# Kernel optimization log

Hardware: AMD Instinct MI355X
Metric: run time of the kernel (lower is better)

## Reference

```python
import jax, jax.numpy as jnp
import numpy as np

NEG_SLOPE = 0.2


def gat_conv(x, src, dst, W, a_src, a_dst, b, num_nodes):
    # x: [N, Fin], W: [Fin, Fout], a_src/a_dst: [Fout], b: [Fout]
    h = x @ W                                   # [N, Fout]
    alpha_s = h @ a_src                         # [N]
    alpha_d = h @ a_dst                         # [N]
    e = alpha_s[src] + alpha_d[dst]             # [E]
    e = jnp.where(e > 0, e, NEG_SLOPE * e)      # LeakyReLU(0.2)
    # segment softmax over edges grouped by destination node
    m = jax.ops.segment_max(e, dst, num_segments=num_nodes)   # [N]
    e = jnp.exp(e - m[dst])
    s = jax.ops.segment_sum(e, dst, num_segments=num_nodes)   # [N]
    alpha = e / s[dst]                          # [E] (every node has a self-loop)
    out = jax.ops.segment_sum(h[src] * alpha[:, None], dst, num_segments=num_nodes)
    return out + b


def setup_inputs() -> dict:
    key = jax.random.key(0)
    ks = jax.random.split(key, 10)
    N, E = 50000, 640000
    Fin, Fh, Fout = 128, 128, 64
    x = jax.random.normal(ks[0], (N, Fin), dtype=jnp.float32)
    edge_index = jax.random.randint(ks[1], (2, E), 0, N, dtype=jnp.int64)
    g = 1.0 / np.sqrt(Fin)
    W1 = jax.random.normal(ks[2], (Fin, Fh), dtype=jnp.float32) * g
    a1_src = jax.random.normal(ks[3], (Fh,), dtype=jnp.float32) * 0.1
    a1_dst = jax.random.normal(ks[4], (Fh,), dtype=jnp.float32) * 0.1
    b1 = jnp.zeros((Fh,), dtype=jnp.float32)
    g2 = 1.0 / np.sqrt(Fh)
    W2 = jax.random.normal(ks[5], (Fh, Fout), dtype=jnp.float32) * g2
    a2_src = jax.random.normal(ks[6], (Fout,), dtype=jnp.float32) * 0.1
    a2_dst = jax.random.normal(ks[7], (Fout,), dtype=jnp.float32) * 0.1
    b2 = jnp.zeros((Fout,), dtype=jnp.float32)
    return {"x": x, "edge_index": edge_index, "W1": W1, "a1_src": a1_src,
            "a1_dst": a1_dst, "b1": b1, "W2": W2, "a2_src": a2_src,
            "a2_dst": a2_dst, "b2": b2}


def reference(x, edge_index, W1, a1_src, a1_dst, b1, W2, a2_src, a2_dst, b2):
    N = x.shape[0]
    loops = jnp.arange(N, dtype=edge_index.dtype)
    src = jnp.concatenate([edge_index[0], loops])  # add self-loops (PyG default)
    dst = jnp.concatenate([edge_index[1], loops])
    h = gat_conv(x, src, dst, W1, a1_src, a1_dst, b1, N)
    h = jax.nn.relu(h)
    # F.dropout(0.1) skipped: deterministic (eval-mode) reference
    out = gat_conv(h, src, dst, W2, a2_src, a2_dst, b2, N)
    return out
```

## Files before the change

kernel.cpp:

```cpp
#include <hip/hip_runtime.h>

#define LEAK 0.2f

static __device__ __forceinline__ float leaky(float e) { return e > 0.f ? e : LEAK * e; }

static __device__ __forceinline__ unsigned f2bf(float f) {
    union { float f; unsigned u; } v; v.f = f;
    return (v.u + 0x7FFFu + ((v.u >> 16) & 1u)) >> 16;
}
static __device__ __forceinline__ float bflo(unsigned u) {
    union { unsigned x; float f; } v; v.x = u << 16; return v.f;
}
static __device__ __forceinline__ float bfhi(unsigned u) {
    union { unsigned x; float f; } v; v.x = u & 0xFFFF0000u; return v.f;
}

using bf16x8 = __attribute__((ext_vector_type(8))) short;
using f32x4 = __attribute__((ext_vector_type(4))) float;

__global__ __launch_bounds__(256) void k_prep(int* __restrict__ counts, int n,
                                              const int* __restrict__ ei, int nwords_check,
                                              int* __restrict__ flag,
                                              const float* __restrict__ W1,
                                              unsigned short* __restrict__ Wt1,
                                              const float* __restrict__ W2,
                                              unsigned short* __restrict__ Wt2, int NB) {
    int bid = blockIdx.x;
    int t = threadIdx.x;
    if (bid == 0) {
        if (t < 64) {
            int bad = 0;
            for (int i = 1 + 2 * t; i < nwords_check; i += 128) bad |= (ei[i] != 0);
            unsigned long long anybad = __ballot(bad != 0);
            if (t == 0) *flag = (anybad == 0ULL) ? 1 : 0;
        }
        return;
    }
    if (bid <= NB) {
        int i = (bid - 1) * 256 + t;
        if (i < n) counts[i] = 0;
        return;
    }
    if (bid <= NB + 4) {
        int q = bid - (NB + 1);
        int c = t & 127, ksub = t >> 7;
        int k0 = q * 32 + ksub * 16;
        union { unsigned short s[16]; uint4 v[2]; } u;
#pragma unroll
        for (int j = 0; j < 16; ++j) u.s[j] = (unsigned short)f2bf(W1[(size_t)(k0 + j) * 128 + c]);
        uint4* dst = (uint4*)(Wt1 + (size_t)c * 128 + k0);
        dst[0] = u.v[0];
        dst[1] = u.v[1];
        return;
    }
    {
        int q = bid - (NB + 5);
        int c = t & 63, ksub = t >> 6;
        int k0 = q * 64 + ksub * 16;
        union { unsigned short s[16]; uint4 v[2]; } u;
#pragma unroll
        for (int j = 0; j < 16; ++j) u.s[j] = (unsigned short)f2bf(W2[(size_t)(k0 + j) * 64 + c]);
        uint4* dst = (uint4*)(Wt2 + (size_t)c * 128 + k0);
        dst[0] = u.v[0];
        dst[1] = u.v[1];
        return;
    }
}

__global__ __launch_bounds__(256) void k_rank(const int* __restrict__ ei,
                                              const int* __restrict__ flag,
                                              int* __restrict__ counts,
                                              int* __restrict__ rankd,
                                              int* __restrict__ srcv, int E) {
    int base = (blockIdx.x * 256 + threadIdx.x) * 4;
    if (base >= E) return;
    int is64 = *flag;
    if (base + 3 < E) {
        int s0, s1, s2, s3, d0, d1, d2, d3;
        if (is64) {
            const uint4* ps = (const uint4*)(ei + 2 * (size_t)base);
            uint4 a = ps[0], b = ps[1];
            const uint4* pd = (const uint4*)(ei + 2 * ((size_t)E + base));
            uint4 c = pd[0], e4 = pd[1];
            s0 = a.x; s1 = a.z; s2 = b.x; s3 = b.z;
            d0 = c.x; d1 = c.z; d2 = e4.x; d3 = e4.z;
        } else {
            int4 a = *(const int4*)(ei + base);
            int4 b = *(const int4*)(ei + (size_t)E + base);
            s0 = a.x; s1 = a.y; s2 = a.z; s3 = a.w;
            d0 = b.x; d1 = b.y; d2 = b.z; d3 = b.w;
        }
        int r0 = atomicAdd(&counts[d0], 1);
        int r1 = atomicAdd(&counts[d1], 1);
        int r2 = atomicAdd(&counts[d2], 1);
        int r3 = atomicAdd(&counts[d3], 1);
        *(int4*)(rankd + base) = make_int4((r0 << 16) | d0, (r1 << 16) | d1,
                                           (r2 << 16) | d2, (r3 << 16) | d3);
        *(int4*)(srcv + base) = make_int4(s0, s1, s2, s3);
    } else {
        for (int j = 0; j < 4 && base + j < E; ++j) {
            int e = base + j;
            int ss = is64 ? ei[2 * (size_t)e] : ei[e];
            int dd = is64 ? ei[2 * ((size_t)E + e)] : ei[(size_t)E + e];
            int r = atomicAdd(&counts[dd], 1);
            rankd[e] = (r << 16) | dd;
            srcv[e] = ss;
        }
    }
}

__global__ void k_scan1(const int* __restrict__ counts, int* __restrict__ incl,
                        int* __restrict__ bsums, int n) {
    __shared__ int s[256];
    int t = threadIdx.x;
    int g = blockIdx.x * 256 + t;
    int v = (g < n) ? counts[g] : 0;
    s[t] = v;
    __syncthreads();
    for (int off = 1; off < 256; off <<= 1) {
        int add = (t >= off) ? s[t - off] : 0;
        __syncthreads();
        s[t] += add;
        __syncthreads();
    }
    if (g < n) incl[g] = s[t];
    if (t == 255) bsums[blockIdx.x] = s[255];
}

__global__ void k_scan2(int* __restrict__ bsums, int nb) {
    __shared__ int s[256];
    int t = threadIdx.x;
    int v = (t < nb) ? bsums[t] : 0;
    s[t] = v;
    __syncthreads();
    for (int off = 1; off < 256; off <<= 1) {
        int add = (t >= off) ? s[t - off] : 0;
        __syncthreads();
        s[t] += add;
        __syncthreads();
    }
    int excl = (t == 0) ? 0 : s[t - 1];
    if (t < nb) bsums[t] = excl;
}

__global__ void k_scan3(const int* __restrict__ incl, const int* __restrict__ bsums,
                        int* __restrict__ rowptr, int n) {
    int g = blockIdx.x * 256 + threadIdx.x;
    if (g < n) rowptr[g + 1] = incl[g] + bsums[blockIdx.x];
    if (g == 0) rowptr[0] = 0;
}

template <int F, bool AF32>
__global__ __launch_bounds__(256) void k_gemm_mfma(const void* __restrict__ Xv,
                                                   const unsigned short* __restrict__ Wt,
                                                   const float* __restrict__ asrc,
                                                   const float* __restrict__ adst,
                                                   unsigned short* __restrict__ Hb,
                                                   float* __restrict__ out_s,
                                                   float* __restrict__ out_d, int n,
                                                   int rowTiles,
                                                   const int* __restrict__ rankd,
                                                   const int* __restrict__ srcv,
                                                   const int* __restrict__ rowptr,
                                                   int* __restrict__ colv, int E) {
    constexpr int K = 128;
    constexpr int KP = K + 8;
    constexpr int NT = F / 16;
    __shared__ unsigned short wsT[F * KP];
    int t = threadIdx.x;

    if (blockIdx.x >= rowTiles) {
        int base = ((blockIdx.x - rowTiles) * 256 + t) * 4;
        if (base >= E) return;
        if (base + 3 < E) {
            int4 rd = *(const int4*)(rankd + base);
            int4 sv = *(const int4*)(srcv + base);
            int p0 = rowptr[rd.x & 0xFFFF] + (rd.x >> 16);
            int p1 = rowptr[rd.y & 0xFFFF] + (rd.y >> 16);
            int p2 = rowptr[rd.z & 0xFFFF] + (rd.z >> 16);
            int p3 = rowptr[rd.w & 0xFFFF] + (rd.w >> 16);
            colv[p0] = sv.x;
            colv[p1] = sv.y;
            colv[p2] = sv.z;
            colv[p3] = sv.w;
        } else {
            for (int j = 0; j < 4 && base + j < E; ++j) {
                int e = base + j;
                int rd = rankd[e];
                colv[rowptr[rd & 0xFFFF] + (rd >> 16)] = srcv[e];
            }
        }
        return;
    }

    int w = t >> 6, lane = t & 63;
    int lrow = lane & 15, kg = lane >> 4;
    long long row0 = (long long)blockIdx.x * 64;

#pragma unroll
    for (int i = t; i < F * (K / 8); i += 256) {
        int c = i / (K / 8), j8 = i % (K / 8);
        uint4 v = ((const uint4*)(Wt + (size_t)c * K))[j8];
        *(uint4*)&wsT[c * KP + 8 * j8] = v;
    }
    __syncthreads();

    long long grow = row0 + w * 16 + lrow;
    bool rowok = grow < n;

    f32x4 acc[NT];
#pragma unroll
    for (int i = 0; i < NT; ++i) acc[i] = (f32x4){0.f, 0.f, 0.f, 0.f};

#pragma unroll
    for (int ks = 0; ks < K / 32; ++ks) {
        bf16x8 af;
        if constexpr (AF32) {
            const float* Xp = (const float*)Xv + grow * K + ks * 32 + kg * 8;
            float4 x0 = make_float4(0.f, 0.f, 0.f, 0.f), x1 = x0;
            if (rowok) {
                x0 = ((const float4*)Xp)[0];
                x1 = ((const float4*)Xp)[1];
            }
            af = (bf16x8){(short)f2bf(x0.x), (short)f2bf(x0.y), (short)f2bf(x0.z), (short)f2bf(x0.w),
                          (short)f2bf(x1.x), (short)f2bf(x1.y), (short)f2bf(x1.z), (short)f2bf(x1.w)};
        } else {
            uint4 u = make_uint4(0, 0, 0, 0);
            if (rowok) {
                const unsigned short* Xp = (const unsigned short*)Xv + grow * K + ks * 32 + kg * 8;
                u = *(const uint4*)Xp;
            }
            af = *(bf16x8*)&u;
        }
#pragma unroll
        for (int nt = 0; nt < NT; ++nt) {
            const unsigned short* bp = &wsT[(nt * 16 + lrow) * KP + ks * 32 + kg * 8];
            uint4 ub = *(const uint4*)bp;
            bf16x8 bf = *(bf16x8*)&ub;
            acc[nt] = __builtin_amdgcn_mfma_f32_16x16x32_bf16(af, bf, acc[nt], 0, 0, 0);
        }
    }

    {
        float ps[4] = {0.f, 0.f, 0.f, 0.f}, pd[4] = {0.f, 0.f, 0.f, 0.f};
#pragma unroll
        for (int nt = 0; nt < NT; ++nt) {
            float asv = asrc[nt * 16 + lrow];
            float adv = adst[nt * 16 + lrow];
#pragma unroll
            for (int i = 0; i < 4; ++i) {
                ps[i] = fmaf(acc[nt][i], asv, ps[i]);
                pd[i] = fmaf(acc[nt][i], adv, pd[i]);
            }
        }
#pragma unroll
        for (int off = 1; off < 16; off <<= 1) {
#pragma unroll
            for (int i = 0; i < 4; ++i) {
                ps[i] += __shfl_xor(ps[i], off);
                pd[i] += __shfl_xor(pd[i], off);
            }
        }
        if (lrow == 0) {
#pragma unroll
            for (int i = 0; i < 4; ++i) {
                long long r = row0 + w * 16 + kg * 4 + i;
                if (r < n) {
                    out_s[r] = ps[i];
                    out_d[r] = pd[i];
                }
            }
        }
    }

    int r0 = w * 16 + kg * 4;
#pragma unroll
    for (int nt = 0; nt < NT; ++nt) {
        int c = nt * 16 + lrow;
#pragma unroll
        for (int i = 0; i < 4; ++i) {
            long long r = row0 + r0 + i;
            if (r < n) Hb[r * F + c] = (unsigned short)f2bf(acc[nt][i]);
        }
    }
}

template <int F, bool RELU, bool OB>
__global__ __launch_bounds__(256) void k_agg(const int* __restrict__ rowptr,
                                             const int* __restrict__ colv,
                                             const float* __restrict__ as_,
                                             const float* __restrict__ ad_,
                                             const unsigned* __restrict__ Hu,
                                             const float* __restrict__ bias,
                                             void* __restrict__ OUT, int n) {
    constexpr int FG8 = F / 8;
    constexpr int GRP = 64 / FG8;
    int node = blockIdx.x * 4 + (threadIdx.x >> 6);
    int lane = threadIdx.x & 63;
    if (node >= n) return;
    int rs = rowptr[node], re = rowptr[node + 1];
    int deg = re - rs;
    float adi = ad_[node];
    float e_self = leaky(as_[node] + adi);

    int scol = node;
    float e_l = -3.0e38f;
    if (lane < deg) {
        scol = colv[rs + lane];
        e_l = leaky(as_[scol] + adi);
    }
    float m = fmaxf(e_l, e_self);
    for (int base = 64; base < deg; base += 64) {
        if (base + lane < deg) m = fmaxf(m, leaky(as_[colv[rs + base + lane]] + adi));
    }
#pragma unroll
    for (int off = 32; off; off >>= 1) m = fmaxf(m, __shfl_xor(m, off));

    float p_l = (lane < deg) ? __expf(e_l - m) : 0.f;
    float ssum = p_l;
    for (int base = 64; base < deg; base += 64) {
        if (base + lane < deg) ssum += __expf(leaky(as_[colv[rs + base + lane]] + adi) - m);
    }
#pragma unroll
    for (int off = 32; off; off >>= 1) ssum += __shfl_xor(ssum, off);
    float pself = __expf(e_self - m);
    ssum += pself;
    float inv = 1.f / ssum;
    float w_l = p_l * inv;
    float wself = pself * inv;

    int grp = lane / FG8;
    int fg = lane % FG8;
    const uint4* __restrict__ H16 = (const uint4*)Hu;
    float a0, a1, a2, a3, a4, a5, a6, a7;
    {
        uint4 hv = H16[(size_t)node * FG8 + fg];
        float ws0 = (grp == 0) ? wself : 0.f;
        a0 = ws0 * bflo(hv.x); a1 = ws0 * bfhi(hv.x);
        a2 = ws0 * bflo(hv.y); a3 = ws0 * bfhi(hv.y);
        a4 = ws0 * bflo(hv.z); a5 = ws0 * bfhi(hv.z);
        a6 = ws0 * bflo(hv.w); a7 = ws0 * bfhi(hv.w);
    }

    int cnt = deg < 64 ? deg : 64;
    constexpr int STEP = 4 * GRP;
    int cntr = (cnt + STEP - 1) / STEP * STEP;
#pragma unroll 1
    for (int i = 0; i < cntr; i += STEP) {
        int i0 = i + grp, i1 = i + GRP + grp, i2 = i + 2 * GRP + grp, i3 = i + 3 * GRP + grp;
        int s0 = __shfl(scol, i0), s1 = __shfl(scol, i1);
        int s2 = __shfl(scol, i2), s3 = __shfl(scol, i3);
        float w0 = __shfl(w_l, i0), w1 = __shfl(w_l, i1);
        float w2 = __shfl(w_l, i2), w3 = __shfl(w_l, i3);
        uint4 g0 = H16[(size_t)s0 * FG8 + fg];
        uint4 g1 = H16[(size_t)s1 * FG8 + fg];
        uint4 g2 = H16[(size_t)s2 * FG8 + fg];
        uint4 g3 = H16[(size_t)s3 * FG8 + fg];
        a0 = fmaf(w0, bflo(g0.x), a0); a1 = fmaf(w0, bfhi(g0.x), a1);
        a2 = fmaf(w0, bflo(g0.y), a2); a3 = fmaf(w0, bfhi(g0.y), a3);
        a4 = fmaf(w0, bflo(g0.z), a4); a5 = fmaf(w0, bfhi(g0.z), a5);
        a6 = fmaf(w0, bflo(g0.w), a6); a7 = fmaf(w0, bfhi(g0.w), a7);
        a0 = fmaf(w1, bflo(g1.x), a0); a1 = fmaf(w1, bfhi(g1.x), a1);
        a2 = fmaf(w1, bflo(g1.y), a2); a3 = fmaf(w1, bfhi(g1.y), a3);
        a4 = fmaf(w1, bflo(g1.z), a4); a5 = fmaf(w1, bfhi(g1.z), a5);
        a6 = fmaf(w1, bflo(g1.w), a6); a7 = fmaf(w1, bfhi(g1.w), a7);
        a0 = fmaf(w2, bflo(g2.x), a0); a1 = fmaf(w2, bfhi(g2.x), a1);
        a2 = fmaf(w2, bflo(g2.y), a2); a3 = fmaf(w2, bfhi(g2.y), a3);
        a4 = fmaf(w2, bflo(g2.z), a4); a5 = fmaf(w2, bfhi(g2.z), a5);
        a6 = fmaf(w2, bflo(g2.w), a6); a7 = fmaf(w2, bfhi(g2.w), a7);
        a0 = fmaf(w3, bflo(g3.x), a0); a1 = fmaf(w3, bfhi(g3.x), a1);
        a2 = fmaf(w3, bflo(g3.y), a2); a3 = fmaf(w3, bfhi(g3.y), a3);
        a4 = fmaf(w3, bflo(g3.z), a4); a5 = fmaf(w3, bfhi(g3.z), a5);
        a6 = fmaf(w3, bflo(g3.w), a6); a7 = fmaf(w3, bfhi(g3.w), a7);
    }
    for (int j = rs + 64; j < re; ++j) {
        int s = colv[j];
        float w = __expf(leaky(as_[s] + adi) - m) * inv;
        float we = (grp == 0) ? w : 0.f;
        uint4 g = H16[(size_t)s * FG8 + fg];
        a0 = fmaf(we, bflo(g.x), a0); a1 = fmaf(we, bfhi(g.x), a1);
        a2 = fmaf(we, bflo(g.y), a2); a3 = fmaf(we, bfhi(g.y), a3);
        a4 = fmaf(we, bflo(g.z), a4); a5 = fmaf(we, bfhi(g.z), a5);
        a6 = fmaf(we, bflo(g.w), a6); a7 = fmaf(we, bfhi(g.w), a7);
    }
#pragma unroll
    for (int off = FG8; off < 64; off <<= 1) {
        a0 += __shfl_xor(a0, off); a1 += __shfl_xor(a1, off);
        a2 += __shfl_xor(a2, off); a3 += __shfl_xor(a3, off);
        a4 += __shfl_xor(a4, off); a5 += __shfl_xor(a5, off);
        a6 += __shfl_xor(a6, off); a7 += __shfl_xor(a7, off);
    }
    if (grp == 0) {
        const float4* b4 = (const float4*)bias;
        float4 bv0 = b4[fg * 2], bv1 = b4[fg * 2 + 1];
        a0 += bv0.x; a1 += bv0.y; a2 += bv0.z; a3 += bv0.w;
        a4 += bv1.x; a5 += bv1.y; a6 += bv1.z; a7 += bv1.w;
        if (RELU) {
            a0 = fmaxf(a0, 0.f); a1 = fmaxf(a1, 0.f);
            a2 = fmaxf(a2, 0.f); a3 = fmaxf(a3, 0.f);
            a4 = fmaxf(a4, 0.f); a5 = fmaxf(a5, 0.f);
            a6 = fmaxf(a6, 0.f); a7 = fmaxf(a7, 0.f);
        }
        if (OB) {
            uint4 p;
            p.x = f2bf(a0) | (f2bf(a1) << 16);
            p.y = f2bf(a2) | (f2bf(a3) << 16);
            p.z = f2bf(a4) | (f2bf(a5) << 16);
            p.w = f2bf(a6) | (f2bf(a7) << 16);
            ((uint4*)OUT)[(size_t)node * FG8 + fg] = p;
        } else {
            float4* o4 = (float4*)((float*)OUT + (size_t)node * F + fg * 8);
            o4[0] = make_float4(a0, a1, a2, a3);
            o4[1] = make_float4(a4, a5, a6, a7);
        }
    }
}

extern "C" void kernel_launch(void* const* d_in, const int* in_sizes, int n_in,
                              void* d_out, int out_size, void* d_ws, size_t ws_size,
                              hipStream_t stream) {
    const float* x   = (const float*)d_in[0];
    const int*   ei  = (const int*)d_in[1];
    const float* W1  = (const float*)d_in[2];
    const float* a1s = (const float*)d_in[3];
    const float* a1d = (const float*)d_in[4];
    const float* b1  = (const float*)d_in[5];
    const float* W2  = (const float*)d_in[6];
    const float* a2s = (const float*)d_in[7];
    const float* a2d = (const float*)d_in[8];
    const float* b2  = (const float*)d_in[9];
    float* out = (float*)d_out;

    int N = in_sizes[0] / 128;
    int E = in_sizes[1] / 2;

    size_t off = 0;
    auto alloc = [&](size_t bytes) -> void* {
        off = (off + 255) & ~(size_t)255;
        void* p = (char*)d_ws + off;
        off += bytes;
        return p;
    };
    unsigned short* h = (unsigned short*)alloc((size_t)N * 128 * 2);
    unsigned short* out1b = (unsigned short*)alloc((size_t)N * 128 * 2);
    unsigned short* Wt1 = (unsigned short*)alloc(128 * 128 * 2);
    unsigned short* Wt2 = (unsigned short*)alloc(64 * 128 * 2);
    float* as_    = (float*)alloc((size_t)N * 4);
    float* ad_    = (float*)alloc((size_t)N * 4);
    int* counts   = (int*)alloc((size_t)N * 4);
    int* rowptr   = (int*)alloc((size_t)(N + 1) * 4);
    int* incl     = (int*)alloc((size_t)N * 4);
    int* bsums    = (int*)alloc(1024);
    int* colv     = (int*)alloc((size_t)E * 4);
    int* rankd    = (int*)alloc((size_t)E * 4);
    int* srcv     = (int*)alloc((size_t)E * 4);
    int* flag     = (int*)alloc(256);

    int NB = (N + 255) / 256;
    int blocksN4 = (N + 3) / 4;
    int rowTiles = (N + 63) / 64;
    int blocksE4 = (E + 1023) / 1024;

    int nchk = 2 * E < 512 ? 2 * E : 512;
    k_prep<<<NB + 7, 256, 0, stream>>>(counts, N, ei, nchk, flag, W1, Wt1, W2, Wt2, NB);
    k_rank<<<blocksE4, 256, 0, stream>>>(ei, flag, counts, rankd, srcv, E);
    k_scan1<<<NB, 256, 0, stream>>>(counts, incl, bsums, N);
    k_scan2<<<1, 256, 0, stream>>>(bsums, NB);
    k_scan3<<<NB, 256, 0, stream>>>(incl, bsums, rowptr, N);

    k_gemm_mfma<128, true><<<rowTiles + blocksE4, 256, 0, stream>>>(
        x, Wt1, a1s, a1d, h, as_, ad_, N, rowTiles, rankd, srcv, rowptr, colv, E);
    k_agg<128, true, true><<<blocksN4, 256, 0, stream>>>(rowptr, colv, as_, ad_,
                                                         (const unsigned*)h, b1, out1b, N);

    k_gemm_mfma<64, false><<<rowTiles, 256, 0, stream>>>(
        out1b, Wt2, a2s, a2d, h, as_, ad_, N, rowTiles, rankd, srcv, rowptr, colv, 0);
    k_agg<64, false, false><<<blocksN4, 256, 0, stream>>>(rowptr, colv, as_, ad_,
                                                          (const unsigned*)h, b2, out, N);
}
```

Baseline: 135.4 us.

## Fuse layer-1 aggregation with layer-2 GEMM and merge scan kernels

Adds a kernel that does the layer-1 attention softmax and neighbor aggregation for 64 nodes per block, writes the ReLU'd bf16 rows into LDS, and runs the layer-2 MFMA GEMM and attention projections from there. This drops the global round trip of the intermediate 128-wide features and one kernel launch. It also folds scan2 and scan3 into one kernel in which every block rescans the block sums redundantly. The cost is less aggregation parallelism: each wave walks 16 nodes serially, and a grid of only about 782 blocks may hide gather latency poorly.

```diff
diff --git a/kernel.cpp b/kernel.cpp
--- a/kernel.cpp
+++ b/kernel.cpp
@@ -127,7 +127,8 @@
     if (t == 255) bsums[blockIdx.x] = s[255];
 }
 
-__global__ void k_scan2(int* __restrict__ bsums, int nb) {
+__global__ void k_scan23(const int* __restrict__ incl, const int* __restrict__ bsums,
+                         int* __restrict__ rowptr, int n, int nb) {
     __shared__ int s[256];
     int t = threadIdx.x;
     int v = (t < nb) ? bsums[t] : 0;
@@ -139,14 +140,9 @@
         s[t] += add;
         __syncthreads();
     }
-    int excl = (t == 0) ? 0 : s[t - 1];
-    if (t < nb) bsums[t] = excl;
-}
-
-__global__ void k_scan3(const int* __restrict__ incl, const int* __restrict__ bsums,
-                        int* __restrict__ rowptr, int n) {
-    int g = blockIdx.x * 256 + threadIdx.x;
-    if (g < n) rowptr[g + 1] = incl[g] + bsums[blockIdx.x];
+    int pre = (blockIdx.x == 0) ? 0 : s[blockIdx.x - 1];
+    int g = blockIdx.x * 256 + t;
+    if (g < n) rowptr[g + 1] = incl[g] + pre;
     if (g == 0) rowptr[0] = 0;
 }
 
@@ -281,6 +277,206 @@
         for (int i = 0; i < 4; ++i) {
             long long r = row0 + r0 + i;
             if (r < n) Hb[r * F + c] = (unsigned short)f2bf(acc[nt][i]);
+        }
+    }
+}
+
+__global__ __launch_bounds__(256) void k_aggemm(const int* __restrict__ rowptr,
+                                                const int* __restrict__ colv,
+                                                const float* __restrict__ as_,
+                                                const float* __restrict__ ad_,
+                                                const unsigned* __restrict__ Hu,
+                                                const float* __restrict__ bias,
+                                                const unsigned short* __restrict__ Wt2,
+                                                const float* __restrict__ a2s,
+                                                const float* __restrict__ a2d,
+                                                unsigned short* __restrict__ H2,
+                                                float* __restrict__ out_s2,
+                                                float* __restrict__ out_d2, int n) {
+    constexpr int K = 128, KP = K + 8;
+    __shared__ unsigned short At[64 * KP];
+    __shared__ unsigned short Wt[64 * KP];
+    int t = threadIdx.x;
+    int w = t >> 6, lane = t & 63;
+
+#pragma unroll
+    for (int i = t; i < 64 * (K / 8); i += 256) {
+        int c = i / (K / 8), j8 = i % (K / 8);
+        uint4 v = ((const uint4*)(Wt2 + (size_t)c * K))[j8];
+        *(uint4*)&Wt[c * KP + 8 * j8] = v;
+    }
+
+    long long node0 = (long long)blockIdx.x * 64 + w * 16;
+    int grp = lane >> 4;
+    int fg = lane & 15;
+    const uint4* __restrict__ H16 = (const uint4*)Hu;
+
+    for (int ii = 0; ii < 16; ++ii) {
+        long long node = node0 + ii;
+        int ldsrow = w * 16 + ii;
+        if (node >= n) {
+            if (lane < 16) *(uint4*)&At[ldsrow * KP + lane * 8] = make_uint4(0, 0, 0, 0);
+            continue;
+        }
+        int rs = rowptr[node], re = rowptr[node + 1];
+        int deg = re - rs;
+        float adi = ad_[node];
+        float e_self = leaky(as_[node] + adi);
+
+        int scol = (int)node;
+        float e_l = -3.0e38f;
+        if (lane < deg) {
+            scol = colv[rs + lane];
+            e_l = leaky(as_[scol] + adi);
+        }
+        float m = fmaxf(e_l, e_self);
+        for (int base = 64; base < deg; base += 64) {
+            if (base + lane < deg) m = fmaxf(m, leaky(as_[colv[rs + base + lane]] + adi));
+        }
+#pragma unroll
+        for (int off = 32; off; off >>= 1) m = fmaxf(m, __shfl_xor(m, off));
+
+        float p_l = (lane < deg) ? __expf(e_l - m) : 0.f;
+        float ssum = p_l;
+        for (int base = 64; base < deg; base += 64) {
+            if (base + lane < deg) ssum += __expf(leaky(as_[colv[rs + base + lane]] + adi) - m);
+        }
+#pragma unroll
+        for (int off = 32; off; off >>= 1) ssum += __shfl_xor(ssum, off);
+        float pself = __expf(e_self - m);
+        ssum += pself;
+        float inv = 1.f / ssum;
+        float w_l = p_l * inv;
+        float wself = pself * inv;
+
+        float a0, a1, a2, a3, a4, a5, a6, a7;
+        {
+            uint4 hv = H16[node * 16 + fg];
+            float ws0 = (grp == 0) ? wself : 0.f;
+            a0 = ws0 * bflo(hv.x); a1 = ws0 * bfhi(hv.x);
+            a2 = ws0 * bflo(hv.y); a3 = ws0 * bfhi(hv.y);
+            a4 = ws0 * bflo(hv.z); a5 = ws0 * bfhi(hv.z);
+            a6 = ws0 * bflo(hv.w); a7 = ws0 * bfhi(hv.w);
+        }
+        int cnt = deg < 64 ? deg : 64;
+        int cntr = (cnt + 15) & ~15;
+#pragma unroll 1
+        for (int i = 0; i < cntr; i += 16) {
+            int i0 = i + grp, i1 = i + 4 + grp, i2 = i + 8 + grp, i3 = i + 12 + grp;
+            int s0 = __shfl(scol, i0), s1 = __shfl(scol, i1);
+            int s2 = __shfl(scol, i2), s3 = __shfl(scol, i3);
+            float w0 = __shfl(w_l, i0), w1 = __shfl(w_l, i1);
+            float w2 = __shfl(w_l, i2), w3 = __shfl(w_l, i3);
+            uint4 g0 = H16[(size_t)s0 * 16 + fg];
+            uint4 g1 = H16[(size_t)s1 * 16 + fg];
+            uint4 g2 = H16[(size_t)s2 * 16 + fg];
+            uint4 g3 = H16[(size_t)s3 * 16 + fg];
+            a0 = fmaf(w0, bflo(g0.x), a0); a1 = fmaf(w0, bfhi(g0.x), a1);
+            a2 = fmaf(w0, bflo(g0.y), a2); a3 = fmaf(w0, bfhi(g0.y), a3);
+            a4 = fmaf(w0, bflo(g0.z), a4); a5 = fmaf(w0, bfhi(g0.z), a5);
+            a6 = fmaf(w0, bflo(g0.w), a6); a7 = fmaf(w0, bfhi(g0.w), a7);
+            a0 = fmaf(w1, bflo(g1.x), a0); a1 = fmaf(w1, bfhi(g1.x), a1);
+            a2 = fmaf(w1, bflo(g1.y), a2); a3 = fmaf(w1, bfhi(g1.y), a3);
+            a4 = fmaf(w1, bflo(g1.z), a4); a5 = fmaf(w1, bfhi(g1.z), a5);
+            a6 = fmaf(w1, bflo(g1.w), a6); a7 = fmaf(w1, bfhi(g1.w), a7);
+            a0 = fmaf(w2, bflo(g2.x), a0); a1 = fmaf(w2, bfhi(g2.x), a1);
+            a2 = fmaf(w2, bflo(g2.y), a2); a3 = fmaf(w2, bfhi(g2.y), a3);
+            a4 = fmaf(w2, bflo(g2.z), a4); a5 = fmaf(w2, bfhi(g2.z), a5);
+            a6 = fmaf(w2, bflo(g2.w), a6); a7 = fmaf(w2, bfhi(g2.w), a7);
+            a0 = fmaf(w3, bflo(g3.x), a0); a1 = fmaf(w3, bfhi(g3.x), a1);
+            a2 = fmaf(w3, bflo(g3.y), a2); a3 = fmaf(w3, bfhi(g3.y), a3);
+            a4 = fmaf(w3, bflo(g3.z), a4); a5 = fmaf(w3, bfhi(g3.z), a5);
+            a6 = fmaf(w3, bflo(g3.w), a6); a7 = fmaf(w3, bfhi(g3.w), a7);
+        }
+        for (int j = rs + 64; j < re; ++j) {
+            int s = colv[j];
+            float ww = __expf(leaky(as_[s] + adi) - m) * inv;
+            float we = (grp == 0) ? ww : 0.f;
+            uint4 g = H16[(size_t)s * 16 + fg];
+            a0 = fmaf(we, bflo(g.x), a0); a1 = fmaf(we, bfhi(g.x), a1);
+            a2 = fmaf(we, bflo(g.y), a2); a3 = fmaf(we, bfhi(g.y), a3);
+            a4 = fmaf(we, bflo(g.z), a4); a5 = fmaf(we, bfhi(g.z), a5);
+            a6 = fmaf(we, bflo(g.w), a6); a7 = fmaf(we, bfhi(g.w), a7);
+        }
+#pragma unroll
+        for (int off = 16; off < 64; off <<= 1) {
+            a0 += __shfl_xor(a0, off); a1 += __shfl_xor(a1, off);
+            a2 += __shfl_xor(a2, off); a3 += __shfl_xor(a3, off);
+            a4 += __shfl_xor(a4, off); a5 += __shfl_xor(a5, off);
+            a6 += __shfl_xor(a6, off); a7 += __shfl_xor(a7, off);
+        }
+        if (grp == 0) {
+            const float4* b4 = (const float4*)bias;
+            float4 bv0 = b4[fg * 2], bv1 = b4[fg * 2 + 1];
+            a0 = fmaxf(a0 + bv0.x, 0.f); a1 = fmaxf(a1 + bv0.y, 0.f);
+            a2 = fmaxf(a2 + bv0.z, 0.f); a3 = fmaxf(a3 + bv0.w, 0.f);
+            a4 = fmaxf(a4 + bv1.x, 0.f); a5 = fmaxf(a5 + bv1.y, 0.f);
+            a6 = fmaxf(a6 + bv1.z, 0.f); a7 = fmaxf(a7 + bv1.w, 0.f);
+            uint4 p;
+            p.x = f2bf(a0) | (f2bf(a1) << 16);
+            p.y = f2bf(a2) | (f2bf(a3) << 16);
+            p.z = f2bf(a4) | (f2bf(a5) << 16);
+            p.w = f2bf(a6) | (f2bf(a7) << 16);
+            *(uint4*)&At[ldsrow * KP + fg * 8] = p;
+        }
+    }
+    __syncthreads();
+
+    int lrow = lane & 15, kg = lane >> 4;
+    long long row0 = (long long)blockIdx.x * 64;
+    f32x4 acc[4];
+#pragma unroll
+    for (int i = 0; i < 4; ++i) acc[i] = (f32x4){0.f, 0.f, 0.f, 0.f};
+#pragma unroll
+    for (int ks = 0; ks < 4; ++ks) {
+        uint4 ua = *(const uint4*)&At[(w * 16 + lrow) * KP + ks * 32 + kg * 8];
+        bf16x8 af = *(bf16x8*)&ua;
+#pragma unroll
+        for (int nt = 0; nt < 4; ++nt) {
+            uint4 ub = *(const uint4*)&Wt[(nt * 16 + lrow) * KP + ks * 32 + kg * 8];
+            bf16x8 bf = *(bf16x8*)&ub;
+            acc[nt] = __builtin_amdgcn_mfma_f32_16x16x32_bf16(af, bf, acc[nt], 0, 0, 0);
+        }
+    }
+    {
+        float ps[4] = {0.f, 0.f, 0.f, 0.f}, pd[4] = {0.f, 0.f, 0.f, 0.f};
+#pragma unroll
+        for (int nt = 0; nt < 4; ++nt) {
+            float asv = a2s[nt * 16 + lrow];
+            float adv = a2d[nt * 16 + lrow];
+#pragma unroll
+            for (int i = 0; i < 4; ++i) {
+                ps[i] = fmaf(acc[nt][i], asv, ps[i]);
+                pd[i] = fmaf(acc[nt][i], adv, pd[i]);
+            }
+        }
+#pragma unroll
+        for (int off = 1; off < 16; off <<= 1) {
+#pragma unroll
+            for (int i = 0; i < 4; ++i) {
+                ps[i] += __shfl_xor(ps[i], off);
+                pd[i] += __shfl_xor(pd[i], off);
+            }
+        }
+        if (lrow == 0) {
+#pragma unroll
+            for (int i = 0; i < 4; ++i) {
+                long long r = row0 + w * 16 + kg * 4 + i;
+                if (r < n) {
+                    out_s2[r] = ps[i];
+                    out_d2[r] = pd[i];
+                }
+            }
+        }
+    }
+    int r0 = w * 16 + kg * 4;
+#pragma unroll
+    for (int nt = 0; nt < 4; ++nt) {
+        int c = nt * 16 + lrow;
+#pragma unroll
+        for (int i = 0; i < 4; ++i) {
+            long long r = row0 + r0 + i;
+            if (r < n) H2[r * 64 + c] = (unsigned short)f2bf(acc[nt][i]);
         }
     }
 }
@@ -441,12 +637,14 @@
         off += bytes;
         return p;
     };
-    unsigned short* h = (unsigned short*)alloc((size_t)N * 128 * 2);
-    unsigned short* out1b = (unsigned short*)alloc((size_t)N * 128 * 2);
+    unsigned short* h  = (unsigned short*)alloc((size_t)N * 128 * 2);
+    unsigned short* h2 = (unsigned short*)alloc((size_t)N * 64 * 2);
     unsigned short* Wt1 = (unsigned short*)alloc(128 * 128 * 2);
     unsigned short* Wt2 = (unsigned short*)alloc(64 * 128 * 2);
     float* as_    = (float*)alloc((size_t)N * 4);
     float* ad_    = (float*)alloc((size_t)N * 4);
+    float* as2    = (float*)alloc((size_t)N * 4);
+    float* ad2    = (float*)alloc((size_t)N * 4);
     int* counts   = (int*)alloc((size_t)N * 4);
     int* rowptr   = (int*)alloc((size_t)(N + 1) * 4);
     int* incl     = (int*)alloc((size_t)N * 4);
@@ -465,16 +663,14 @@
     k_prep<<<NB + 7, 256, 0, stream>>>(counts, N, ei, nchk, flag, W1, Wt1, W2, Wt2, NB);
     k_rank<<<blocksE4, 256, 0, stream>>>(ei, flag, counts, rankd, srcv, E);
     k_scan1<<<NB, 256, 0, stream>>>(counts, incl, bsums, N);
-    k_scan2<<<1, 256, 0, stream>>>(bsums, NB);
-    k_scan3<<<NB, 256, 0, stream>>>(incl, bsums, rowptr, N);
+    k_scan23<<<NB, 256, 0, stream>>>(incl, bsums, rowptr, N, NB);
 
     k_gemm_mfma<128, true><<<rowTiles + blocksE4, 256, 0, stream>>>(
         x, Wt1, a1s, a1d, h, as_, ad_, N, rowTiles, rankd, srcv, rowptr, colv, E);
-    k_agg<128, true, true><<<blocksN4, 256, 0, stream>>>(rowptr, colv, as_, ad_,
-                                                         (const unsigned*)h, b1, out1b, N);
-
-    k_gemm_mfma<64, false><<<rowTiles, 256, 0, stream>>>(
-        out1b, Wt2, a2s, a2d, h, as_, ad_, N, rowTiles, rankd, srcv, rowptr, colv, 0);
-    k_agg<64, false, false><<<blocksN4, 256, 0, stream>>>(rowptr, colv, as_, ad_,
-                                                          (const unsigned*)h, b2, out, N);
-}
+
+    k_aggemm<<<rowTiles, 256, 0, stream>>>(rowptr, colv, as_, ad_, (const unsigned*)h,
+                                           b1, Wt2, a2s, a2d, h2, as2, ad2, N);
+
+    k_agg<64, false, false><<<blocksN4, 256, 0, stream>>>(rowptr, colv, as2, ad2,
+                                                          (const unsigned*)h2, b2, out, N);
+}
```

After: 145.4 us. 7.4% more time.

## Process two destination nodes per wavefront in aggregation and merge scan passes

Applied to the files above, without the earlier changes.

The aggregation kernel now has each 64-lane wavefront handle two destination nodes at once. Their softmax reductions and neighbour gathers are interleaved, so more independent memory loads are in flight per wave and the per-node setup is amortised. The second and third scan kernels are fused: every block redundantly scans the block sums itself, which removes one launch. In exchange the aggregation kernel uses about twice the accumulator registers, which may lower occupancy, and lanes can sit idle when the two nodes have very different degrees.

```diff
diff --git a/kernel.cpp b/kernel.cpp
--- a/kernel.cpp
+++ b/kernel.cpp
@@ -17,6 +17,12 @@
 
 using bf16x8 = __attribute__((ext_vector_type(8))) short;
 using f32x4 = __attribute__((ext_vector_type(4))) float;
+
+#define FMA8(A0, A1, A2, A3, A4, A5, A6, A7, W, G)              \
+    A0 = fmaf(W, bflo(G.x), A0); A1 = fmaf(W, bfhi(G.x), A1);   \
+    A2 = fmaf(W, bflo(G.y), A2); A3 = fmaf(W, bfhi(G.y), A3);   \
+    A4 = fmaf(W, bflo(G.z), A4); A5 = fmaf(W, bfhi(G.z), A5);   \
+    A6 = fmaf(W, bflo(G.w), A6); A7 = fmaf(W, bfhi(G.w), A7);
 
 __global__ __launch_bounds__(256) void k_prep(int* __restrict__ counts, int n,
                                               const int* __restrict__ ei, int nwords_check,
@@ -127,7 +133,8 @@
     if (t == 255) bsums[blockIdx.x] = s[255];
 }
 
-__global__ void k_scan2(int* __restrict__ bsums, int nb) {
+__global__ void k_scan23(const int* __restrict__ incl, const int* __restrict__ bsums,
+                         int* __restrict__ rowptr, int n, int nb) {
     __shared__ int s[256];
     int t = threadIdx.x;
     int v = (t < nb) ? bsums[t] : 0;
@@ -139,14 +146,9 @@
         s[t] += add;
         __syncthreads();
     }
-    int excl = (t == 0) ? 0 : s[t - 1];
-    if (t < nb) bsums[t] = excl;
-}
-
-__global__ void k_scan3(const int* __restrict__ incl, const int* __restrict__ bsums,
-                        int* __restrict__ rowptr, int n) {
-    int g = blockIdx.x * 256 + threadIdx.x;
-    if (g < n) rowptr[g + 1] = incl[g] + bsums[blockIdx.x];
+    int pre = (blockIdx.x == 0) ? 0 : s[blockIdx.x - 1];
+    int g = blockIdx.x * 256 + t;
+    if (g < n) rowptr[g + 1] = incl[g] + pre;
     if (g == 0) rowptr[0] = 0;
 }
 
@@ -295,123 +297,190 @@
                                              void* __restrict__ OUT, int n) {
     constexpr int FG8 = F / 8;
     constexpr int GRP = 64 / FG8;
-    int node = blockIdx.x * 4 + (threadIdx.x >> 6);
+    constexpr int STEP = 4 * GRP;
+    int wid = blockIdx.x * 4 + (threadIdx.x >> 6);
     int lane = threadIdx.x & 63;
-    if (node >= n) return;
-    int rs = rowptr[node], re = rowptr[node + 1];
-    int deg = re - rs;
-    float adi = ad_[node];
-    float e_self = leaky(as_[node] + adi);
-
-    int scol = node;
-    float e_l = -3.0e38f;
-    if (lane < deg) {
-        scol = colv[rs + lane];
-        e_l = leaky(as_[scol] + adi);
-    }
-    float m = fmaxf(e_l, e_self);
-    for (int base = 64; base < deg; base += 64) {
-        if (base + lane < deg) m = fmaxf(m, leaky(as_[colv[rs + base + lane]] + adi));
-    }
-#pragma unroll
-    for (int off = 32; off; off >>= 1) m = fmaxf(m, __shfl_xor(m, off));
-
-    float p_l = (lane < deg) ? __expf(e_l - m) : 0.f;
-    float ssum = p_l;
-    for (int base = 64; base < deg; base += 64) {
-        if (base + lane < deg) ssum += __expf(leaky(as_[colv[rs + base + lane]] + adi) - m);
-    }
-#pragma unroll
-    for (int off = 32; off; off >>= 1) ssum += __shfl_xor(ssum, off);
-    float pself = __expf(e_self - m);
-    ssum += pself;
-    float inv = 1.f / ssum;
-    float w_l = p_l * inv;
-    float wself = pself * inv;
+    long long nA = (long long)wid * 2;
+    if (nA >= n) return;
+    long long nB = nA + 1;
+    bool vB = nB < n;
+    long long nBc = vB ? nB : nA;
+
+    int rsA = rowptr[nA], reA = rowptr[nA + 1];
+    int rsB = rowptr[nBc], reB = rowptr[nBc + 1];
+    int degA = reA - rsA, degB = reB - rsB;
+    float adiA = ad_[nA], adiB = ad_[nBc];
+    float esA = leaky(as_[nA] + adiA);
+    float esB = leaky(as_[nBc] + adiB);
+
+    int scA = (int)nA, scB = (int)nBc;
+    float eA = -3.0e38f, eB = -3.0e38f;
+    if (lane < degA) scA = colv[rsA + lane];
+    if (lane < degB) scB = colv[rsB + lane];
+    if (lane < degA) eA = leaky(as_[scA] + adiA);
+    if (lane < degB) eB = leaky(as_[scB] + adiB);
+
+    float mA = fmaxf(eA, esA), mB = fmaxf(eB, esB);
+    for (int base = 64; base < degA; base += 64)
+        if (base + lane < degA) mA = fmaxf(mA, leaky(as_[colv[rsA + base + lane]] + adiA));
+    for (int base = 64; base < degB; base += 64)
+        if (base + lane < degB) mB = fmaxf(mB, leaky(as_[colv[rsB + base + lane]] + adiB));
+#pragma unroll
+    for (int off = 32; off; off >>= 1) {
+        mA = fmaxf(mA, __shfl_xor(mA, off));
+        mB = fmaxf(mB, __shfl_xor(mB, off));
+    }
+
+    float pA = (lane < degA) ? __expf(eA - mA) : 0.f;
+    float pB = (lane < degB) ? __expf(eB - mB) : 0.f;
+    float sA = pA, sB = pB;
+    for (int base = 64; base < degA; base += 64)
+        if (base + lane < degA) sA += __expf(leaky(as_[colv[rsA + base + lane]] + adiA) - mA);
+    for (int base = 64; base < degB; base += 64)
+        if (base + lane < degB) sB += __expf(leaky(as_[colv[rsB + base + lane]] + adiB) - mB);
+#pragma unroll
+    for (int off = 32; off; off >>= 1) {
+        sA += __shfl_xor(sA, off);
+        sB += __shfl_xor(sB, off);
+    }
+    float psA = __expf(esA - mA), psB = __expf(esB - mB);
+    sA += psA;
+    sB += psB;
+    float invA = 1.f / sA, invB = 1.f / sB;
+    float wA = pA * invA, wB = pB * invB;
+    float wsA = psA * invA, wsB = psB * invB;
 
     int grp = lane / FG8;
     int fg = lane % FG8;
     const uint4* __restrict__ H16 = (const uint4*)Hu;
-    float a0, a1, a2, a3, a4, a5, a6, a7;
+    float a0A, a1A, a2A, a3A, a4A, a5A, a6A, a7A;
+    float a0B, a1B, a2B, a3B, a4B, a5B, a6B, a7B;
     {
-        uint4 hv = H16[(size_t)node * FG8 + fg];
-        float ws0 = (grp == 0) ? wself : 0.f;
-        a0 = ws0 * bflo(hv.x); a1 = ws0 * bfhi(hv.x);
-        a2 = ws0 * bflo(hv.y); a3 = ws0 * bfhi(hv.y);
-        a4 = ws0 * bflo(hv.z); a5 = ws0 * bfhi(hv.z);
-        a6 = ws0 * bflo(hv.w); a7 = ws0 * bfhi(hv.w);
-    }
-
-    int cnt = deg < 64 ? deg : 64;
-    constexpr int STEP = 4 * GRP;
-    int cntr = (cnt + STEP - 1) / STEP * STEP;
+        uint4 hvA = H16[(size_t)nA * FG8 + fg];
+        uint4 hvB = H16[(size_t)nBc * FG8 + fg];
+        float w0A = (grp == 0) ? wsA : 0.f;
+        float w0B = (grp == 0) ? wsB : 0.f;
+        a0A = w0A * bflo(hvA.x); a1A = w0A * bfhi(hvA.x);
+        a2A = w0A * bflo(hvA.y); a3A = w0A * bfhi(hvA.y);
+        a4A = w0A * bflo(hvA.z); a5A = w0A * bfhi(hvA.z);
+        a6A = w0A * bflo(hvA.w); a7A = w0A * bfhi(hvA.w);
+        a0B = w0B * bflo(hvB.x); a1B = w0B * bfhi(hvB.x);
+        a2B = w0B * bflo(hvB.y); a3B = w0B * bfhi(hvB.y);
+        a4B = w0B * bflo(hvB.z); a5B = w0B * bfhi(hvB.z);
+        a6B = w0B * bflo(hvB.w); a7B = w0B * bfhi(hvB.w);
+    }
+
+    int cntA = degA < 64 ? degA : 64;
+    int cntB = degB < 64 ? degB : 64;
+    int cntrA = (cntA + STEP - 1) / STEP * STEP;
+    int cntrB = (cntB + STEP - 1) / STEP * STEP;
+    int cntrM = cntrA > cntrB ? cntrA : cntrB;
 #pragma unroll 1
-    for (int i = 0; i < cntr; i += STEP) {
-        int i0 = i + grp, i1 = i + GRP + grp, i2 = i + 2 * GRP + grp, i3 = i + 3 * GRP + grp;
-        int s0 = __shfl(scol, i0), s1 = __shfl(scol, i1);
-        int s2 = __shfl(scol, i2), s3 = __shfl(scol, i3);
-        float w0 = __shfl(w_l, i0), w1 = __shfl(w_l, i1);
-        float w2 = __shfl(w_l, i2), w3 = __shfl(w_l, i3);
-        uint4 g0 = H16[(size_t)s0 * FG8 + fg];
-        uint4 g1 = H16[(size_t)s1 * FG8 + fg];
-        uint4 g2 = H16[(size_t)s2 * FG8 + fg];
-        uint4 g3 = H16[(size_t)s3 * FG8 + fg];
-        a0 = fmaf(w0, bflo(g0.x), a0); a1 = fmaf(w0, bfhi(g0.x), a1);
-        a2 = fmaf(w0, bflo(g0.y), a2); a3 = fmaf(w0, bfhi(g0.y), a3);
-        a4 = fmaf(w0, bflo(g0.z), a4); a5 = fmaf(w0, bfhi(g0.z), a5);
-        a6 = fmaf(w0, bflo(g0.w), a6); a7 = fmaf(w0, bfhi(g0.w), a7);
-        a0 = fmaf(w1, bflo(g1.x), a0); a1 = fmaf(w1, bfhi(g1.x), a1);
-        a2 = fmaf(w1, bflo(g1.y), a2); a3 = fmaf(w1, bfhi(g1.y), a3);
-        a4 = fmaf(w1, bflo(g1.z), a4); a5 = fmaf(w1, bfhi(g1.z), a5);
-        a6 = fmaf(w1, bflo(g1.w), a6); a7 = fmaf(w1, bfhi(g1.w), a7);
-        a0 = fmaf(w2, bflo(g2.x), a0); a1 = fmaf(w2, bfhi(g2.x), a1);
-        a2 = fmaf(w2, bflo(g2.y), a2); a3 = fmaf(w2, bfhi(g2.y), a3);
-        a4 = fmaf(w2, bflo(g2.z), a4); a5 = fmaf(w2, bfhi(g2.z), a5);
-        a6 = fmaf(w2, bflo(g2.w), a6); a7 = fmaf(w2, bfhi(g2.w), a7);
-        a0 = fmaf(w3, bflo(g3.x), a0); a1 = fmaf(w3, bfhi(g3.x), a1);
-        a2 = fmaf(w3, bflo(g3.y), a2); a3 = fmaf(w3, bfhi(g3.y), a3);
-        a4 = fmaf(w3, bflo(g3.z), a4); a5 = fmaf(w3, bfhi(g3.z), a5);
-        a6 = fmaf(w3, bflo(g3.w), a6); a7 = fmaf(w3, bfhi(g3.w), a7);
-    }
-    for (int j = rs + 64; j < re; ++j) {
+    for (int i = 0; i < cntrM; i += STEP) {
+        bool doA = i < cntrA, doB = i < cntrB;
+        uint4 gA0, gA1, gA2, gA3, gB0, gB1, gB2, gB3;
+        float wA0, wA1, wA2, wA3, wB0, wB1, wB2, wB3;
+        if (doA) {
+            int i0 = i + grp, i1 = i + GRP + grp, i2 = i + 2 * GRP + grp, i3 = i + 3 * GRP + grp;
+            int s0 = __shfl(scA, i0), s1 = __shfl(scA, i1);
+            int s2 = __shfl(scA, i2), s3 = __shfl(scA, i3);
+            wA0 = __shfl(wA, i0); wA1 = __shfl(wA, i1);
+            wA2 = __shfl(wA, i2); wA3 = __shfl(wA, i3);
+            gA0 = H16[(size_t)s0 * FG8 + fg];
+            gA1 = H16[(size_t)s1 * FG8 + fg];
+            gA2 = H16[(size_t)s2 * FG8 + fg];
+            gA3 = H16[(size_t)s3 * FG8 + fg];
+        }
+        if (doB) {
+            int i0 = i + grp, i1 = i + GRP + grp, i2 = i + 2 * GRP + grp, i3 = i + 3 * GRP + grp;
+            int s0 = __shfl(scB, i0), s1 = __shfl(scB, i1);
+            int s2 = __shfl(scB, i2), s3 = __shfl(scB, i3);
+            wB0 = __shfl(wB, i0); wB1 = __shfl(wB, i1);
+            wB2 = __shfl(wB, i2); wB3 = __shfl(wB, i3);
+            gB0 = H16[(size_t)s0 * FG8 + fg];
+            gB1 = H16[(size_t)s1 * FG8 + fg];
+            gB2 = H16[(size_t)s2 * FG8 + fg];
+            gB3 = H16[(size_t)s3 * FG8 + fg];
+        }
+        if (doA) {
+            FMA8(a0A, a1A, a2A, a3A, a4A, a5A, a6A, a7A, wA0, gA0)
+            FMA8(a0A, a1A, a2A, a3A, a4A, a5A, a6A, a7A, wA1, gA1)
+            FMA8(a0A, a1A, a2A, a3A, a4A, a5A, a6A, a7A, wA2, gA2)
+            FMA8(a0A, a1A, a2A, a3A, a4A, a5A, a6A, a7A, wA3, gA3)
+        }
+        if (doB) {
+            FMA8(a0B, a1B, a2B, a3B, a4B, a5B, a6B, a7B, wB0, gB0)
+            FMA8(a0B, a1B, a2B, a3B, a4B, a5B, a6B, a7B, wB1, gB1)
+            FMA8(a0B, a1B, a2B, a3B, a4B, a5B, a6B, a7B, wB2, gB2)
+            FMA8(a0B, a1B, a2B, a3B, a4B, a5B, a6B, a7B, wB3, gB3)
+        }
+    }
+    for (int j = rsA + 64; j < reA; ++j) {
         int s = colv[j];
-        float w = __expf(leaky(as_[s] + adi) - m) * inv;
+        float w = __expf(leaky(as_[s] + adiA) - mA) * invA;
         float we = (grp == 0) ? w : 0.f;
         uint4 g = H16[(size_t)s * FG8 + fg];
-        a0 = fmaf(we, bflo(g.x), a0); a1 = fmaf(we, bfhi(g.x), a1);
-        a2 = fmaf(we, bflo(g.y), a2); a3 = fmaf(we, bfhi(g.y), a3);
-        a4 = fmaf(we, bflo(g.z), a4); a5 = fmaf(we, bfhi(g.z), a5);
-        a6 = fmaf(we, bflo(g.w), a6); a7 = fmaf(we, bfhi(g.w), a7);
+        FMA8(a0A, a1A, a2A, a3A, a4A, a5A, a6A, a7A, we, g)
+    }
+    for (int j = rsB + 64; j < reB; ++j) {
+        int s = colv[j];
+        float w = __expf(leaky(as_[s] + adiB) - mB) * invB;
+        float we = (grp == 0) ? w : 0.f;
+        uint4 g = H16[(size_t)s * FG8 + fg];
+        FMA8(a0B, a1B, a2B, a3B, a4B, a5B, a6B, a7B, we, g)
     }
 #pragma unroll
     for (int off = FG8; off < 64; off <<= 1) {
-        a0 += __shfl_xor(a0, off); a1 += __shfl_xor(a1, off);
-        a2 += __shfl_xor(a2, off); a3 += __shfl_xor(a3, off);
-        a4 += __shfl_xor(a4, off); a5 += __shfl_xor(a5, off);
-        a6 += __shfl_xor(a6, off); a7 += __shfl_xor(a7, off);
+        a0A += __shfl_xor(a0A, off); a1A += __shfl_xor(a1A, off);
+        a2A += __shfl_xor(a2A, off); a3A += __shfl_xor(a3A, off);
+        a4A += __shfl_xor(a4A, off); a5A += __shfl_xor(a5A, off);
+        a6A += __shfl_xor(a6A, off); a7A += __shfl_xor(a7A, off);
+        a0B += __shfl_xor(a0B, off); a1B += __shfl_xor(a1B, off);
+        a2B += __shfl_xor(a2B, off); a3B += __shfl_xor(a3B, off);
+        a4B += __shfl_xor(a4B, off); a5B += __shfl_xor(a5B, off);
+        a6B += __shfl_xor(a6B, off); a7B += __shfl_xor(a7B, off);
     }
     if (grp == 0) {
         const float4* b4 = (const float4*)bias;
         float4 bv0 = b4[fg * 2], bv1 = b4[fg * 2 + 1];
-        a0 += bv0.x; a1 += bv0.y; a2 += bv0.z; a3 += bv0.w;
-        a4 += bv1.x; a5 += bv1.y; a6 += bv1.z; a7 += bv1.w;
+        a0A += bv0.x; a1A += bv0.y; a2A += bv0.z; a3A += bv0.w;
+        a4A += bv1.x; a5A += bv1.y; a6A += bv1.z; a7A += bv1.w;
+        a0B += bv0.x; a1B += bv0.y; a2B += bv0.z; a3B += bv0.w;
+        a4B += bv1.x; a5B += bv1.y; a6B += bv1.z; a7B += bv1.w;
         if (RELU) {
-            a0 = fmaxf(a0, 0.f); a1 = fmaxf(a1, 0.f);
-            a2 = fmaxf(a2, 0.f); a3 = fmaxf(a3, 0.f);
-            a4 = fmaxf(a4, 0.f); a5 = fmaxf(a5, 0.f);
-            a6 = fmaxf(a6, 0.f); a7 = fmaxf(a7, 0.f);
+            a0A = fmaxf(a0A, 0.f); a1A = fmaxf(a1A, 0.f);
+            a2A = fmaxf(a2A, 0.f); a3A = fmaxf(a3A, 0.f);
+            a4A = fmaxf(a4A, 0.f); a5A = fmaxf(a5A, 0.f);
+            a6A = fmaxf(a6A, 0.f); a7A = fmaxf(a7A, 0.f);
+            a0B = fmaxf(a0B, 0.f); a1B = fmaxf(a1B, 0.f);
+            a2B = fmaxf(a2B, 0.f); a3B = fmaxf(a3B, 0.f);
+            a4B = fmaxf(a4B, 0.f); a5B = fmaxf(a5B, 0.f);
+            a6B = fmaxf(a6B, 0.f); a7B = fmaxf(a7B, 0.f);
         }
         if (OB) {
             uint4 p;
-            p.x = f2bf(a0) | (f2bf(a1) << 16);
-            p.y = f2bf(a2) | (f2bf(a3) << 16);
-            p.z = f2bf(a4) | (f2bf(a5) << 16);
-            p.w = f2bf(a6) | (f2bf(a7) << 16);
-            ((uint4*)OUT)[(size_t)node * FG8 + fg] = p;
+            p.x = f2bf(a0A) | (f2bf(a1A) << 16);
+            p.y = f2bf(a2A) | (f2bf(a3A) << 16);
+            p.z = f2bf(a4A) | (f2bf(a5A) << 16);
+            p.w = f2bf(a6A) | (f2bf(a7A) << 16);
+            ((uint4*)OUT)[(size_t)nA * FG8 + fg] = p;
+            if (vB) {
+                uint4 q;
+                q.x = f2bf(a0B) | (f2bf(a1B) << 16);
+                q.y = f2bf(a2B) | (f2bf(a3B) << 16);
+                q.z = f2bf(a4B) | (f2bf(a5B) << 16);
+                q.w = f2bf(a6B) | (f2bf(a7B) << 16);
+                ((uint4*)OUT)[(size_t)nB * FG8 + fg] = q;
+            }
         } else {
-            float4* o4 = (float4*)((float*)OUT + (size_t)node * F + fg * 8);
-            o4[0] = make_float4(a0, a1, a2, a3);
-            o4[1] = make_float4(a4, a5, a6, a7);
+            float4* oA = (float4*)((float*)OUT + (size_t)nA * F + fg * 8);
+            oA[0] = make_float4(a0A, a1A, a2A, a3A);
+            oA[1] = make_float4(a4A, a5A, a6A, a7A);
+            if (vB) {
+                float4* oB = (float4*)((float*)OUT + (size_t)nB * F + fg * 8);
+                oB[0] = make_float4(a0B, a1B, a2B, a3B);
+                oB[1] = make_float4(a4B, a5B, a6B, a7B);
+            }
         }
     }
 }
@@ -457,7 +526,7 @@
     int* flag     = (int*)alloc(256);
 
     int NB = (N + 255) / 256;
-    int blocksN4 = (N + 3) / 4;
+    int blocksN8 = (N + 7) / 8;
     int rowTiles = (N + 63) / 64;
     int blocksE4 = (E + 1023) / 1024;
 
@@ -465,16 +534,15 @@
     k_prep<<<NB + 7, 256, 0, stream>>>(counts, N, ei, nchk, flag, W1, Wt1, W2, Wt2, NB);
     k_rank<<<blocksE4, 256, 0, stream>>>(ei, flag, counts, rankd, srcv, E);
     k_scan1<<<NB, 256, 0, stream>>>(counts, incl, bsums, N);
-    k_scan2<<<1, 256, 0, stream>>>(bsums, NB);
-    k_scan3<<<NB, 256, 0, stream>>>(incl, bsums, rowptr, N);
+    k_scan23<<<NB, 256, 0, stream>>>(incl, bsums, rowptr, N, NB);
 
     k_gemm_mfma<128, true><<<rowTiles + blocksE4, 256, 0, stream>>>(
         x, Wt1, a1s, a1d, h, as_, ad_, N, rowTiles, rankd, srcv, rowptr, colv, E);
-    k_agg<128, true, true><<<blocksN4, 256, 0, stream>>>(rowptr, colv, as_, ad_,
+    k_agg<128, true, true><<<blocksN8, 256, 0, stream>>>(rowptr, colv, as_, ad_,
                                                          (const unsigned*)h, b1, out1b, N);
 
     k_gemm_mfma<64, false><<<rowTiles, 256, 0, stream>>>(
         out1b, Wt2, a2s, a2d, h, as_, ad_, N, rowTiles, rankd, srcv, rowptr, colv, 0);
-    k_agg<64, false, false><<<blocksN4, 256, 0, stream>>>(rowptr, colv, as_, ad_,
+    k_agg<64, false, false><<<blocksN8, 256, 0, stream>>>(rowptr, colv, as_, ad_,
                                                           (const unsigned*)h, b2, out, N);
 }
```

After: 143.2 us. 5.7% more time.
